# Optimization experiments

Hardware: AMD Instinct MI355X
Metric: run time of the kernel (lower is better)

Reference implementation:

```python
import jax, jax.numpy as jnp
import numpy as np


def setup_inputs() -> dict:
    key = jax.random.key(0)
    k1, k2, k3 = jax.random.split(key, 3)
    B, R, Din, D = 4096, 4096, 1024, 1024
    x = jax.random.normal(k1, (B, Din), dtype=jnp.float32)
    refs = jax.random.normal(k2, (R, Din), dtype=jnp.float32)
    W = jax.random.normal(k3, (Din, D), dtype=jnp.float32) * (1.0 / np.sqrt(Din))
    b = jnp.zeros((D,), dtype=jnp.float32)
    return {"x": x, "refs": refs, "W": W, "b": b}


def reference(x, refs, W, b) -> jnp.ndarray:
    # feature extractor (linear stand-in for the CResNet embedding)
    vin = x @ W + b          # (B, D)
    vrefs = refs @ W + b     # (R, D)
    # compute_degradation_metric: mean_r ||vin_b - vref_r||^2
    # = ||vin||^2 + mean_r ||vref_r||^2 - 2 * vin @ mean_r(vref_r)
    # Same math as the naive broadcast-sub-square-sum-mean, GEMM-friendly form.
    sq_in = jnp.sum(vin * vin, axis=1)                 # (B,)
    mean_sq_ref = jnp.mean(jnp.sum(vrefs * vrefs, axis=1))  # scalar
    mean_ref = jnp.mean(vrefs, axis=0)                 # (D,)
    cross = vin @ mean_ref                             # (B,)
    degradation_metric = sq_in + mean_sq_ref - 2.0 * cross
    return degradation_metric
```

## Files before the change

kernel.cpp:

```cpp
#include <hip/hip_runtime.h>
#include <hip/hip_bf16.h>
#include <stdint.h>


typedef __attribute__((ext_vector_type(8))) short short8;
typedef __attribute__((ext_vector_type(4))) float f32x4;

__device__ __forceinline__ short f2bf(float f) {
  uint32_t u = __builtin_bit_cast(uint32_t, f);
  uint32_t r = (u + 0x7fffu + ((u >> 16) & 1u)) >> 16;
  return (short)r;
}
__device__ __forceinline__ float bf2f(short s) {
  uint32_t u = ((uint32_t)(uint16_t)s) << 16;
  return __builtin_bit_cast(float, u);
}

#define WS_XB 0u
#define WS_RB 8388608u
#define WS_WT 16777216u
#define WS_CP 18874368u
#define WS_CS 20971520u
#define WS_TV 20975616u
#define WS_XP 20979712u
#define WS_RR 20996096u

__global__ __launch_bounds__(256) void k_prep(
    const float* __restrict__ x, const float* __restrict__ refs,
    const float* __restrict__ W, short* __restrict__ xb, short* __restrict__ rb,
    short* __restrict__ wt, float* __restrict__ cspart, float* __restrict__ zacc) {
  __shared__ short tile[64][68];
  const int b = blockIdx.x, t = threadIdx.x;
  if (b < 512) {
    for (int i = b * 256 + t; i < 1048576; i += 512 * 256) {
      float4 v = ((const float4*)x)[i];
      uint32_t lo = (uint16_t)f2bf(v.x) | ((uint32_t)(uint16_t)f2bf(v.y) << 16);
      uint32_t hi = (uint16_t)f2bf(v.z) | ((uint32_t)(uint16_t)f2bf(v.w) << 16);
      ((uint2*)xb)[i] = make_uint2(lo, hi);
    }
  } else if (b < 1024) {
    const int rblk = b - 512;
    const int c0 = t * 4;
    float s0 = 0.f, s1 = 0.f, s2 = 0.f, s3 = 0.f;
    for (int r = rblk * 8; r < rblk * 8 + 8; ++r) {
      float4 v = *(const float4*)&refs[(size_t)r * 1024 + c0];
      s0 += v.x; s1 += v.y; s2 += v.z; s3 += v.w;
      uint32_t lo = (uint16_t)f2bf(v.x) | ((uint32_t)(uint16_t)f2bf(v.y) << 16);
      uint32_t hi = (uint16_t)f2bf(v.z) | ((uint32_t)(uint16_t)f2bf(v.w) << 16);
      *(uint2*)&rb[(size_t)r * 1024 + c0] = make_uint2(lo, hi);
    }
    cspart[rblk * 1024 + c0 + 0] = s0;
    cspart[rblk * 1024 + c0 + 1] = s1;
    cspart[rblk * 1024 + c0 + 2] = s2;
    cspart[rblk * 1024 + c0 + 3] = s3;
  } else if (b < 1280) {
    const int tb = b - 1024;
    const int tk = (tb >> 4) * 64, tn = (tb & 15) * 64;
    const int kk = t >> 4, nn4 = (t & 15) * 4;
#pragma unroll
    for (int p = 0; p < 4; ++p) {
      int k = kk + p * 16;
      float4 v = *(const float4*)&W[(size_t)(tk + k) * 1024 + tn + nn4];
      tile[nn4 + 0][k] = f2bf(v.x);
      tile[nn4 + 1][k] = f2bf(v.y);
      tile[nn4 + 2][k] = f2bf(v.z);
      tile[nn4 + 3][k] = f2bf(v.w);
    }
    __syncthreads();
    const int nn = t >> 4, kk4 = (t & 15) * 4;
#pragma unroll
    for (int p = 0; p < 4; ++p) {
      int n = nn + p * 16;
      uint32_t lo = (uint16_t)tile[n][kk4 + 0] | ((uint32_t)(uint16_t)tile[n][kk4 + 1] << 16);
      uint32_t hi = (uint16_t)tile[n][kk4 + 2] | ((uint32_t)(uint16_t)tile[n][kk4 + 3] << 16);
      *(uint2*)&wt[(size_t)(tn + n) * 1024 + tk + kk4] = make_uint2(lo, hi);
    }
  } else {
    const int i = (b - 1280) * 256 + t;
    ((float4*)zacc)[i]        = make_float4(0.f, 0.f, 0.f, 0.f);
    ((float4*)zacc)[i + 1024] = make_float4(0.f, 0.f, 0.f, 0.f);
  }
}

__global__ void k_colsum(const float* __restrict__ cspart, float* __restrict__ colsum) {
  __shared__ float sh[8][32];
  const int t = threadIdx.x;
  const int c = t & 31, pg = t >> 5;
  const int k = blockIdx.x * 32 + c;
  float s = 0.f;
  for (int i = 0; i < 64; ++i) s += cspart[(size_t)(pg * 64 + i) * 1024 + k];
  sh[pg][c] = s;
  __syncthreads();
  if (t < 32) {
    float tot = 0.f;
#pragma unroll
    for (int g = 0; g < 8; ++g) tot += sh[g][t];
    colsum[blockIdx.x * 32 + t] = tot;
  }
}

__global__ void k_tvec(const short* __restrict__ Wt, const float* __restrict__ colsum,
                       const float* __restrict__ bias, float* __restrict__ tv) {
  int w = threadIdx.x >> 6, l = threadIdx.x & 63;
  int n = blockIdx.x * 4 + w;
  float s = 0.f;
  for (int k = l; k < 1024; k += 64)
    s += colsum[k] * (1.0f / 4096.0f) * bf2f(Wt[(size_t)n * 1024 + k]);
#pragma unroll
  for (int off = 32; off; off >>= 1) s += __shfl_down(s, off, 64);
  if (l == 0) tv[n] = s + bias[n];
}

__global__ __launch_bounds__(512) void k_main(
    const short* __restrict__ Xb, const short* __restrict__ Rb,
    const short* __restrict__ Wt, const float* __restrict__ bias,
    const float* __restrict__ tv, float* __restrict__ xpart,
    float* __restrict__ refrow) {
  __shared__ __align__(16) short As[2][128 * 64];
  __shared__ __align__(16) short Bs[2][128 * 64];
  const int t = threadIdx.x;
  const int w = t >> 6, l = t & 63;
  const int wr = w >> 2, wc = w & 3;
  const int bx = blockIdx.x;
  const int nt = bx >> 6;
  const int mt = bx & 63;
  const bool is_x = (mt < 32);
  const short* Am = is_x ? Xb : Rb;
  const int m0 = (is_x ? mt : (mt - 32)) * 128;
  const int n0 = nt * 128;

  const int srow = t >> 3;
  const int sslot = t & 7;

  f32x4 acc[4][2] = {};

  auto stage = [&](int buf, int kt) {
    const int k0 = kt * 64;
#pragma unroll
    for (int issue = 0; issue < 2; ++issue) {
      const int row = srow + issue * 64;
      const int sg = sslot ^ (row & 7);
      const short* ga = Am + ((size_t)(m0 + row) * 1024 + k0 + sg * 8);
      const short* gb = Wt + ((size_t)(n0 + row) * 1024 + k0 + sg * 8);
      char* la = (char*)&As[buf][0] + issue * 8192 + w * 1024;
      char* lb = (char*)&Bs[buf][0] + issue * 8192 + w * 1024;
      __builtin_amdgcn_global_load_lds(
          (const __attribute__((address_space(1))) unsigned int*)ga,
          (__attribute__((address_space(3))) unsigned int*)la, 16, 0, 0);
      __builtin_amdgcn_global_load_lds(
          (const __attribute__((address_space(1))) unsigned int*)gb,
          (__attribute__((address_space(3))) unsigned int*)lb, 16, 0, 0);
    }
  };

  stage(0, 0);
  stage(1, 1);

  for (int kt = 0; kt < 16; ++kt) {
    if (kt < 15) asm volatile("s_waitcnt vmcnt(4)" ::: "memory");
    else         asm volatile("s_waitcnt vmcnt(0)" ::: "memory");
    __builtin_amdgcn_s_barrier();
    const int cur = kt & 1;
#pragma unroll
    for (int kk = 0; kk < 2; ++kk) {
      short8 af[4], bfr[2];
#pragma unroll
      for (int i = 0; i < 4; ++i) {
        const int ra = wr * 64 + i * 16 + (l & 15);
        const int s = (l >> 4) + kk * 4;
        af[i] = *(const short8*)&As[cur][ra * 64 + ((s ^ (ra & 7)) * 8)];
      }
#pragma unroll
      for (int j = 0; j < 2; ++j) {
        const int rbw = wc * 32 + j * 16 + (l & 15);
        const int s = (l >> 4) + kk * 4;
        bfr[j] = *(const short8*)&Bs[cur][rbw * 64 + ((s ^ (rbw & 7)) * 8)];
      }
      __builtin_amdgcn_s_setprio(1);
#pragma unroll
      for (int i = 0; i < 4; ++i)
#pragma unroll
        for (int j = 0; j < 2; ++j)
          acc[i][j] = __builtin_amdgcn_mfma_f32_16x16x32_bf16(af[i], bfr[j], acc[i][j], 0, 0, 0);
      __builtin_amdgcn_s_setprio(0);
    }
    __builtin_amdgcn_s_barrier();
    if (kt + 2 < 16) stage(cur, kt + 2);
  }

  float bv[2], tvv[2];
#pragma unroll
  for (int n2 = 0; n2 < 2; ++n2) {
    const int col = n0 + wc * 32 + n2 * 16 + (l & 15);
    bv[n2] = bias[col];
    tvv[n2] = tv[col];
  }
#pragma unroll
  for (int m4 = 0; m4 < 4; ++m4) {
#pragma unroll
    for (int j = 0; j < 4; ++j) {
      float sq = 0.f, cr = 0.f;
#pragma unroll
      for (int n2 = 0; n2 < 2; ++n2) {
        const float v = acc[m4][n2][j] + bv[n2];
        sq += v * v;
        cr += v * tvv[n2];
      }
#pragma unroll
      for (int off = 1; off < 16; off <<= 1) {
        sq += __shfl_xor(sq, off, 64);
        cr += __shfl_xor(cr, off, 64);
      }
      if ((l & 15) == 0) {
        const int rm = m0 + wr * 64 + m4 * 16 + (l >> 4) * 4 + j;
        if (is_x) atomicAdd(&xpart[rm], sq - 2.0f * cr);
        else      atomicAdd(&refrow[rm], sq);
      }
    }
  }
}

__global__ void k_tail(const float* __restrict__ refrow, const float* __restrict__ xpart,
                       float* __restrict__ out) {
  __shared__ float sh[16];
  const int t = threadIdx.x;
  float s = 0.f;
  for (int i = t; i < 4096; i += 1024) s += refrow[i];
#pragma unroll
  for (int off = 32; off; off >>= 1) s += __shfl_down(s, off, 64);
  const int w = t >> 6, l = t & 63;
  if (l == 0) sh[w] = s;
  __syncthreads();
  if (t == 0) {
    float tot = 0.f;
#pragma unroll
    for (int i = 0; i < 16; ++i) tot += sh[i];
    sh[0] = tot * (1.0f / 4096.0f);
  }
  __syncthreads();
  const float ms = sh[0];
  for (int i = t; i < 4096; i += 1024) out[i] = xpart[i] + ms;
}

extern "C" void kernel_launch(void* const* d_in, const int* in_sizes, int n_in,
                              void* d_out, int out_size, void* d_ws, size_t ws_size,
                              hipStream_t stream) {
  const float* x    = (const float*)d_in[0];
  const float* refs = (const float*)d_in[1];
  const float* W    = (const float*)d_in[2];
  const float* bias = (const float*)d_in[3];
  float* out = (float*)d_out;
  char* ws = (char*)d_ws;

  short* xb     = (short*)(ws + WS_XB);
  short* rb     = (short*)(ws + WS_RB);
  short* wt     = (short*)(ws + WS_WT);
  float* cspart = (float*)(ws + WS_CP);
  float* colsum = (float*)(ws + WS_CS);
  float* tvv    = (float*)(ws + WS_TV);
  float* xpart  = (float*)(ws + WS_XP);
  float* refrow = (float*)(ws + WS_RR);

  hipLaunchKernelGGL(k_prep, dim3(1284), dim3(256), 0, stream, x, refs, W, xb, rb, wt, cspart, xpart);
  hipLaunchKernelGGL(k_colsum, dim3(32), dim3(256), 0, stream, cspart, colsum);
  hipLaunchKernelGGL(k_tvec, dim3(256), dim3(256), 0, stream, wt, colsum, bias, tvv);
  hipLaunchKernelGGL(k_main, dim3(512), dim3(512), 0, stream, xb, rb, wt, bias, tvv, xpart, refrow);
  hipLaunchKernelGGL(k_tail, dim3(1), dim3(1024), 0, stream, refrow, xpart, out);
}
```

Measured before the change: 51.44 us.

## Fuse fp32-to-bf16 conversion of activations into the GEMM A-operand load path

The prep kernel no longer converts x and refs into bf16 workspace copies. The main GEMM now loads fp32 A tiles into registers one step ahead, packs them to bf16 with v_cvt_pk_bf16_f32, and writes them into swizzled LDS. W still arrives through async global-to-LDS loads. This removes a full read-convert-write pass over both activation matrices and its extra kernel work. In exchange the GEMM reads twice the A bytes per tile, which are re-read across N tiles. It also adds register pressure, under a new occupancy hint, and relies on compiler-inserted waits for the async B loads.

```diff
diff --git a/kernel.cpp b/kernel.cpp
--- a/kernel.cpp
+++ b/kernel.cpp
@@ -16,8 +16,6 @@
   return __builtin_bit_cast(float, u);
 }
 
-#define WS_XB 0u
-#define WS_RB 8388608u
 #define WS_WT 16777216u
 #define WS_CP 18874368u
 #define WS_CS 20971520u
@@ -26,35 +24,24 @@
 #define WS_RR 20996096u
 
 __global__ __launch_bounds__(256) void k_prep(
-    const float* __restrict__ x, const float* __restrict__ refs,
-    const float* __restrict__ W, short* __restrict__ xb, short* __restrict__ rb,
+    const float* __restrict__ refs, const float* __restrict__ W,
     short* __restrict__ wt, float* __restrict__ cspart, float* __restrict__ zacc) {
   __shared__ short tile[64][68];
   const int b = blockIdx.x, t = threadIdx.x;
   if (b < 512) {
-    for (int i = b * 256 + t; i < 1048576; i += 512 * 256) {
-      float4 v = ((const float4*)x)[i];
-      uint32_t lo = (uint16_t)f2bf(v.x) | ((uint32_t)(uint16_t)f2bf(v.y) << 16);
-      uint32_t hi = (uint16_t)f2bf(v.z) | ((uint32_t)(uint16_t)f2bf(v.w) << 16);
-      ((uint2*)xb)[i] = make_uint2(lo, hi);
-    }
-  } else if (b < 1024) {
-    const int rblk = b - 512;
+    const int rblk = b;
     const int c0 = t * 4;
     float s0 = 0.f, s1 = 0.f, s2 = 0.f, s3 = 0.f;
     for (int r = rblk * 8; r < rblk * 8 + 8; ++r) {
       float4 v = *(const float4*)&refs[(size_t)r * 1024 + c0];
       s0 += v.x; s1 += v.y; s2 += v.z; s3 += v.w;
-      uint32_t lo = (uint16_t)f2bf(v.x) | ((uint32_t)(uint16_t)f2bf(v.y) << 16);
-      uint32_t hi = (uint16_t)f2bf(v.z) | ((uint32_t)(uint16_t)f2bf(v.w) << 16);
-      *(uint2*)&rb[(size_t)r * 1024 + c0] = make_uint2(lo, hi);
     }
     cspart[rblk * 1024 + c0 + 0] = s0;
     cspart[rblk * 1024 + c0 + 1] = s1;
     cspart[rblk * 1024 + c0 + 2] = s2;
     cspart[rblk * 1024 + c0 + 3] = s3;
-  } else if (b < 1280) {
-    const int tb = b - 1024;
+  } else if (b < 768) {
+    const int tb = b - 512;
     const int tk = (tb >> 4) * 64, tn = (tb & 15) * 64;
     const int kk = t >> 4, nn4 = (t & 15) * 4;
 #pragma unroll
@@ -76,7 +63,7 @@
       *(uint2*)&wt[(size_t)(tn + n) * 1024 + tk + kk4] = make_uint2(lo, hi);
     }
   } else {
-    const int i = (b - 1280) * 256 + t;
+    const int i = (b - 768) * 256 + t;
     ((float4*)zacc)[i]        = make_float4(0.f, 0.f, 0.f, 0.f);
     ((float4*)zacc)[i + 1024] = make_float4(0.f, 0.f, 0.f, 0.f);
   }
@@ -111,8 +98,8 @@
   if (l == 0) tv[n] = s + bias[n];
 }
 
-__global__ __launch_bounds__(512) void k_main(
-    const short* __restrict__ Xb, const short* __restrict__ Rb,
+__global__ __launch_bounds__(512, 4) void k_main(
+    const float* __restrict__ X, const float* __restrict__ R,
     const short* __restrict__ Wt, const float* __restrict__ bias,
     const float* __restrict__ tv, float* __restrict__ xpart,
     float* __restrict__ refrow) {
@@ -125,40 +112,60 @@
   const int nt = bx >> 6;
   const int mt = bx & 63;
   const bool is_x = (mt < 32);
-  const short* Am = is_x ? Xb : Rb;
+  const float* Am = is_x ? X : R;
   const int m0 = (is_x ? mt : (mt - 32)) * 128;
   const int n0 = nt * 128;
 
   const int srow = t >> 3;
   const int sslot = t & 7;
+  const int arow = t >> 4;
+  const int acol = (t & 15) * 4;
+  const int asl = (t & 15) >> 1, ah = t & 1;
 
   f32x4 acc[4][2] = {};
-
-  auto stage = [&](int buf, int kt) {
+  float4 areg[4];
+
+  auto stageB = [&](int buf, int kt) {
     const int k0 = kt * 64;
 #pragma unroll
     for (int issue = 0; issue < 2; ++issue) {
       const int row = srow + issue * 64;
       const int sg = sslot ^ (row & 7);
-      const short* ga = Am + ((size_t)(m0 + row) * 1024 + k0 + sg * 8);
       const short* gb = Wt + ((size_t)(n0 + row) * 1024 + k0 + sg * 8);
-      char* la = (char*)&As[buf][0] + issue * 8192 + w * 1024;
       char* lb = (char*)&Bs[buf][0] + issue * 8192 + w * 1024;
-      __builtin_amdgcn_global_load_lds(
-          (const __attribute__((address_space(1))) unsigned int*)ga,
-          (__attribute__((address_space(3))) unsigned int*)la, 16, 0, 0);
       __builtin_amdgcn_global_load_lds(
           (const __attribute__((address_space(1))) unsigned int*)gb,
           (__attribute__((address_space(3))) unsigned int*)lb, 16, 0, 0);
     }
   };
-
-  stage(0, 0);
-  stage(1, 1);
+  auto loadA = [&](int kt) {
+    const int k0 = kt * 64;
+#pragma unroll
+    for (int i = 0; i < 4; ++i) {
+      const int r = arow + i * 32;
+      areg[i] = *(const float4*)&Am[(size_t)(m0 + r) * 1024 + k0 + acol];
+    }
+  };
+  auto writeA = [&](int buf) {
+#pragma unroll
+    for (int i = 0; i < 4; ++i) {
+      const int r = arow + i * 32;
+      uint32_t lo, hi;
+      asm("v_cvt_pk_bf16_f32 %0, %1, %2" : "=v"(lo) : "v"(areg[i].x), "v"(areg[i].y));
+      asm("v_cvt_pk_bf16_f32 %0, %1, %2" : "=v"(hi) : "v"(areg[i].z), "v"(areg[i].w));
+      char* p = (char*)&As[buf][0] + r * 128 + (((asl ^ (r & 7)) * 16) + ah * 8);
+      *(uint2*)p = make_uint2(lo, hi);
+    }
+  };
+
+  stageB(0, 0);
+  stageB(1, 1);
+  loadA(0);
+  writeA(0);
+  loadA(1);
 
   for (int kt = 0; kt < 16; ++kt) {
-    if (kt < 15) asm volatile("s_waitcnt vmcnt(4)" ::: "memory");
-    else         asm volatile("s_waitcnt vmcnt(0)" ::: "memory");
+    asm volatile("s_waitcnt lgkmcnt(0)" ::: "memory");
     __builtin_amdgcn_s_barrier();
     const int cur = kt & 1;
 #pragma unroll
@@ -185,7 +192,9 @@
       __builtin_amdgcn_s_setprio(0);
     }
     __builtin_amdgcn_s_barrier();
-    if (kt + 2 < 16) stage(cur, kt + 2);
+    if (kt + 2 < 16) stageB(cur, kt + 2);
+    if (kt + 1 < 16) writeA((kt + 1) & 1);
+    if (kt + 2 < 16) loadA(kt + 2);
   }
 
   float bv[2], tvv[2];
@@ -252,8 +261,6 @@
   float* out = (float*)d_out;
   char* ws = (char*)d_ws;
 
-  short* xb     = (short*)(ws + WS_XB);
-  short* rb     = (short*)(ws + WS_RB);
   short* wt     = (short*)(ws + WS_WT);
   float* cspart = (float*)(ws + WS_CP);
   float* colsum = (float*)(ws + WS_CS);
@@ -261,9 +268,9 @@
   float* xpart  = (float*)(ws + WS_XP);
   float* refrow = (float*)(ws + WS_RR);
 
-  hipLaunchKernelGGL(k_prep, dim3(1284), dim3(256), 0, stream, x, refs, W, xb, rb, wt, cspart, xpart);
+  hipLaunchKernelGGL(k_prep, dim3(772), dim3(256), 0, stream, refs, W, wt, cspart, xpart);
   hipLaunchKernelGGL(k_colsum, dim3(32), dim3(256), 0, stream, cspart, colsum);
   hipLaunchKernelGGL(k_tvec, dim3(256), dim3(256), 0, stream, wt, colsum, bias, tvv);
-  hipLaunchKernelGGL(k_main, dim3(512), dim3(512), 0, stream, xb, rb, wt, bias, tvv, xpart, refrow);
+  hipLaunchKernelGGL(k_main, dim3(512), dim3(512), 0, stream, x, refs, wt, bias, tvv, xpart, refrow);
   hipLaunchKernelGGL(k_tail, dim3(1), dim3(1024), 0, stream, refrow, xpart, out);
 }
```

Measured after the change: 51.80 us. No clear change (+0.7%).
